# Performance work log

Measured on AMD Instinct MI355X. Metric: run time of the kernel, lower is better.

The kernel has to match this reference:

```python
import jax, jax.numpy as jnp
import numpy as np

TOP_K = 8
NUM_EXPERTS = 256
NUM_GROUPS = 8
TOPK_GROUP = 4
SCALE = 2.5
EPS = 1e-20


def setup_inputs() -> dict:
    key = jax.random.key(0)
    k1, k2, k3 = jax.random.split(key, 3)
    T, H = 8192, 7168
    hidden_states = jax.random.normal(k1, (T, H), dtype=jnp.float32)
    # scale ~ kaiming-ish so logits are O(1) and sigmoid is not saturated
    weight = jax.random.normal(k2, (NUM_EXPERTS, H), dtype=jnp.float32) * (H ** -0.5)
    e_score_correction_bias = jax.random.normal(k3, (NUM_EXPERTS,), dtype=jnp.float32) * 0.1
    return {"hidden_states": hidden_states, "weight": weight,
            "e_score_correction_bias": e_score_correction_bias}


def reference(hidden_states, weight, e_score_correction_bias):
    T = hidden_states.shape[0]
    epg = NUM_EXPERTS // NUM_GROUPS  # experts per group
    # gating logits: [T, E]
    logits = jnp.einsum('th,eh->te', hidden_states.astype(jnp.float32),
                        weight.astype(jnp.float32))
    scores = jax.nn.sigmoid(logits)
    scores_for_choice = scores + e_score_correction_bias[None, :]
    # group score = sum of top-2 corrected scores within each group: [T, G]
    grouped = scores_for_choice.reshape(T, NUM_GROUPS, epg)
    top2, _ = jax.lax.top_k(grouped, 2)
    group_scores = top2.sum(axis=-1)
    # select topk_group groups, build mask [T, G]
    _, group_idx = jax.lax.top_k(group_scores, TOPK_GROUP)
    group_mask = jnp.zeros((T, NUM_GROUPS), dtype=scores.dtype)
    group_mask = group_mask.at[jnp.arange(T)[:, None], group_idx].set(1.0)
    # expand to expert mask [T, E]
    score_mask = jnp.repeat(group_mask, epg, axis=1)
    tmp_scores = jnp.where(score_mask > 0, scores_for_choice, 0.0)
    # top_k experts among allowed groups
    _, topk_idx = jax.lax.top_k(tmp_scores, TOP_K)
    # gather UNcorrected scores as weights
    topk_weight = jnp.take_along_axis(scores, topk_idx, axis=1)
    topk_weight = topk_weight / (topk_weight.sum(axis=-1, keepdims=True) + EPS)
    topk_weight = topk_weight * SCALE
    return topk_idx, topk_weight
```

## Files before the change

### kernel.cpp

```cpp
#include <hip/hip_runtime.h>
#include <cmath>

typedef __attribute__((ext_vector_type(8))) _Float16 half8;
typedef __attribute__((ext_vector_type(8))) unsigned short ushort8;
typedef __attribute__((ext_vector_type(4))) float f32x4;

#define HH 7168
#define NE 256
#define NQ 224
#define NITER 112
#define TOPK 8
#define TOPKG 4
#define WSC 1024.f
#define INV_WS (1.f/1024.f)
#define C1 (1.f/2048.f)
#define C2 (1.f/4194304.f)

__device__ __forceinline__ void split2(float x, unsigned short& h, unsigned short& m){
  const _Float16 hh = (_Float16)x;
  const float r = x - (float)hh;
  const _Float16 mm = (_Float16)(r * 2048.f);
  h = __builtin_bit_cast(unsigned short, hh);
  m = __builtin_bit_cast(unsigned short, mm);
}

__global__ __launch_bounds__(256) void prep_w(const float* __restrict__ wgt,
                                              unsigned short* __restrict__ bh,
                                              unsigned short* __restrict__ bm){
  const int b = blockIdx.x;
  const int nt = b & 15, qb = (b >> 4) * 4;
  const int w = threadIdx.x >> 6, L = threadIdx.x & 63;
  const int q = qb + w;
  const int e = nt*16 + (L & 15);
  const int k0 = 32*q + 8*(L >> 4);
  const float4 a0 = *(const float4*)(wgt + (size_t)e*HH + k0);
  const float4 a1 = *(const float4*)(wgt + (size_t)e*HH + k0 + 4);
  const float v[8] = {a0.x,a0.y,a0.z,a0.w,a1.x,a1.y,a1.z,a1.w};
  ushort8 h8, m8;
#pragma unroll
  for(int j=0;j<8;j++){ unsigned short hh,mm; split2(v[j]*WSC, hh, mm); h8[j]=hh; m8[j]=mm; }
  const size_t base = ((size_t)(q*16+nt)*64 + L)*8;
  *(ushort8*)(bh+base) = h8;
  *(ushort8*)(bm+base) = m8;
}

#define ABYTE(buf,lvl,mt,q,row) ((((((buf)*2+(lvl))*2+(mt))*2+(q))*64+(row))*16)
#define BBYTE(buf,lvl,q,nt) ((((buf)*4+(lvl)*2+(q))*8+(nt))<<10)
__device__ __forceinline__ int swz(int bo){ return bo ^ (((bo >> 8) & 7) << 4); }

__device__ __forceinline__ void glds16(const void* g, void* l){
  __builtin_amdgcn_global_load_lds(
      (const __attribute__((address_space(1))) unsigned int*)g,
      (__attribute__((address_space(3))) unsigned int*)l, 16, 0, 0);
}

__global__ __launch_bounds__(512,4)
void gemm(const float* __restrict__ hs,
          const unsigned short* __restrict__ bhp,
          const unsigned short* __restrict__ bmp,
          float* __restrict__ lgout){
  __shared__ __align__(16) unsigned char blds[65536];
  __shared__ __align__(16) unsigned char alds[16384];

  const int tid = threadIdx.x, lane = tid & 63, w = tid >> 6;
  const int b = blockIdx.x;
  const int slice = (b >> 2) & 1;
  const int tg = (b >> 3)*4 + (b & 3);
  const int tb = tg*32, eb = slice*128;
  const int mtp = w >> 2, ntp = w & 3;

  f32x4 ksum[2], kcmp[2], c0[2], c1[2], c2[2];
#pragma unroll
  for(int c=0;c<2;c++){ ksum[c]=f32x4{0,0,0,0}; kcmp[c]=f32x4{0,0,0,0}; }

  const int tokS = (tid & 255) >> 3, kidx = tid & 7;
  const int mtS = tokS >> 4, m16S = tokS & 15;
  const int qS = kidx >> 2, kgS = kidx & 3;
  const int rowS = kgS*16 + m16S;
  const float* agp = hs + (size_t)(tb + tokS)*HH + kidx*8;

  auto stage = [&](int buf, const float4* g){
    unsigned short h[8], m[8];
    const float* gv = (const float*)g;
#pragma unroll
    for(int p=0;p<8;p++) split2(gv[p], h[p], m[p]);
    ushort8 h8, m8;
#pragma unroll
    for(int j=0;j<8;j++){ h8[j]=h[j]; m8[j]=m[j]; }
    *(ushort8*)&alds[swz(ABYTE(buf,0,mtS,qS,rowS))] = h8;
    *(ushort8*)&alds[swz(ABYTE(buf,1,mtS,qS,rowS))] = m8;
  };

  auto bstage = [&](int buf, int q32base){
#pragma unroll
    for(int j=0;j<4;j++){
      const int sid = w*4 + j;
      const int lvl = sid >> 4, q = (sid >> 3) & 1, nt = sid & 7;
      const int q32 = q32base + q;
      const unsigned short* src = (lvl ? bmp : bhp)
          + ((size_t)((q32*16 + slice*8 + nt)*64 + lane))*8;
      glds16(src, &blds[BBYTE(buf,lvl,q,nt)]);
    }
  };

  float4 ga[2];
  if(tid < 256){
    ga[0] = *(const float4*)(agp);
    ga[1] = *(const float4*)(agp + 4);
  }
  bstage(0, 0);
  if(tid < 256) stage(0, ga);
  __syncthreads();

  for(int i=0;i<NITER;i++){
    const int cur = i & 1, nb = cur ^ 1;
    const bool more = (i+1 < NITER);
    if(more){
      if(tid < 256){
        const float* ap = agp + (size_t)(i+1)*64;
        ga[0] = *(const float4*)(ap);
        ga[1] = *(const float4*)(ap + 4);
      }
      bstage(nb, 2*(i+1));
    }
    if((i & 1) == 0){
#pragma unroll
      for(int c=0;c<2;c++){ c0[c]=f32x4{0,0,0,0}; c1[c]=f32x4{0,0,0,0}; c2[c]=f32x4{0,0,0,0}; }
    }
#pragma unroll
    for(int s=0;s<2;s++){
      const half8 ah = *(const half8*)&alds[swz(ABYTE(cur,0,mtp,s,lane))];
      const half8 am = *(const half8*)&alds[swz(ABYTE(cur,1,mtp,s,lane))];
      half8 Bh[2], Bm[2];
#pragma unroll
      for(int ntl=0;ntl<2;ntl++){
        Bh[ntl] = *(const half8*)&blds[BBYTE(cur,0,s,ntp*2+ntl) + lane*16];
        Bm[ntl] = *(const half8*)&blds[BBYTE(cur,1,s,ntp*2+ntl) + lane*16];
      }
      __builtin_amdgcn_s_setprio(1);
#pragma unroll
      for(int ntl=0;ntl<2;ntl++){
        c0[ntl] = __builtin_amdgcn_mfma_f32_16x16x32_f16(ah, Bh[ntl], c0[ntl], 0,0,0);
        c1[ntl] = __builtin_amdgcn_mfma_f32_16x16x32_f16(ah, Bm[ntl], c1[ntl], 0,0,0);
        c1[ntl] = __builtin_amdgcn_mfma_f32_16x16x32_f16(am, Bh[ntl], c1[ntl], 0,0,0);
        c2[ntl] = __builtin_amdgcn_mfma_f32_16x16x32_f16(am, Bm[ntl], c2[ntl], 0,0,0);
      }
      __builtin_amdgcn_s_setprio(0);
    }
    if(more && tid < 256) stage(nb, ga);
    if(i & 1){
#pragma unroll
      for(int c=0;c<2;c++)
#pragma unroll
        for(int r=0;r<4;r++){
          const float v = c0[c][r] + c1[c][r]*C1 + c2[c][r]*C2;
          const float y = v - kcmp[c][r];
          const float t = ksum[c][r] + y;
          kcmp[c][r] = (t - ksum[c][r]) - y;
          ksum[c][r] = t;
        }
    }
    __syncthreads();
  }

#pragma unroll
  for(int ntl=0;ntl<2;ntl++)
#pragma unroll
    for(int r=0;r<4;r++){
      const int tok = mtp*16 + (lane>>4)*4 + r;
      const int e = (ntp*2+ntl)*16 + (lane&15);
      const float lg = (ksum[ntl][r] - kcmp[ntl][r]) * INV_WS;
      lgout[(size_t)(tb+tok)*NE + eb + e] = lg;
    }
}

__global__ __launch_bounds__(256)
void gate(const float* __restrict__ lg, const float* __restrict__ bias,
          float* __restrict__ out, int T){
  const int tid = threadIdx.x, lane = tid & 63, wv = tid >> 6;
  const int t = blockIdx.x*4 + wv;
  const float4 bias4 = *(const float4*)(bias + 4*lane);
  const int g = lane >> 3;
  const float NEG_INF = -__builtin_inff();

  const float4 l4 = *(const float4*)(lg + (size_t)t*NE + 4*lane);
  float4 r4;
  r4.x = 1.f/(1.f + expf(-l4.x));
  r4.y = 1.f/(1.f + expf(-l4.y));
  r4.z = 1.f/(1.f + expf(-l4.z));
  r4.w = 1.f/(1.f + expf(-l4.w));
  float4 s4;
  s4.x = r4.x + bias4.x; s4.y = r4.y + bias4.y;
  s4.z = r4.z + bias4.z; s4.w = r4.w + bias4.w;

  float m1 = s4.x, m2 = NEG_INF;
  if (s4.y > m1) { m2 = m1; m1 = s4.y; } else if (s4.y > m2) m2 = s4.y;
  if (s4.z > m1) { m2 = m1; m1 = s4.z; } else if (s4.z > m2) m2 = s4.z;
  if (s4.w > m1) { m2 = m1; m1 = s4.w; } else if (s4.w > m2) m2 = s4.w;
#pragma unroll
  for (int m = 1; m <= 4; m <<= 1) {
    const float o1 = __shfl_xor(m1, m);
    const float o2 = __shfl_xor(m2, m);
    const float nm1 = fmaxf(m1, o1);
    const float nm2 = fmaxf(fminf(m1, o1), fmaxf(m2, o2));
    m1 = nm1; m2 = nm2;
  }
  const float gs = m1 + m2;

  float gsv[8];
#pragma unroll
  for (int j = 0; j < 8; ++j) gsv[j] = __shfl(gs, j * 8);

  unsigned gm = 0;
#pragma unroll
  for (int r = 0; r < TOPKG; ++r) {
    float best = NEG_INF; int bj = 0;
#pragma unroll
    for (int j = 0; j < 8; ++j) {
      const bool avail = !((gm >> j) & 1u);
      if (avail && gsv[j] > best) { best = gsv[j]; bj = j; }
    }
    gm |= 1u << bj;
  }
  const bool allowed = (gm >> g) & 1u;

  float v0 = allowed ? s4.x : 0.f;
  float v1 = allowed ? s4.y : 0.f;
  float v2 = allowed ? s4.z : 0.f;
  float v3 = allowed ? s4.w : 0.f;

  float sumw = 0.f;
  int myidx = 0; float myraw = 0.f;
#pragma unroll
  for (int r = 0; r < TOPK; ++r) {
    float bv = v0; int bj = 0;
    if (v1 > bv) { bv = v1; bj = 1; }
    if (v2 > bv) { bv = v2; bj = 2; }
    if (v3 > bv) { bv = v3; bj = 3; }
    int bidx = 4 * lane + bj;
#pragma unroll
    for (int m = 1; m < 64; m <<= 1) {
      const float ov = __shfl_xor(bv, m);
      const int   oi = __shfl_xor(bidx, m);
      if (ov > bv || (ov == bv && oi < bidx)) { bv = ov; bidx = oi; }
    }
    const int oj = bidx & 3;
    const float cand = (oj == 0) ? r4.x
                     : (oj == 1) ? r4.y
                     : (oj == 2) ? r4.z
                     :             r4.w;
    const float raw = __shfl(cand, bidx >> 2);
    sumw += raw;
    if (lane == r) { myidx = bidx; myraw = raw; }
    if (lane == (bidx >> 2)) {
      if      (oj == 0) v0 = NEG_INF;
      else if (oj == 1) v1 = NEG_INF;
      else if (oj == 2) v2 = NEG_INF;
      else              v3 = NEG_INF;
    }
  }

  if (lane < TOPK) {
    out[(size_t)t * TOPK + lane] = (float)myidx;
    out[(size_t)T * TOPK + (size_t)t * TOPK + lane] = myraw / (sumw + 1e-20f) * 2.5f;
  }
}

extern "C" void kernel_launch(void* const* d_in, const int* in_sizes, int n_in,
                              void* d_out, int out_size, void* d_ws, size_t ws_size,
                              hipStream_t stream) {
  const float* hs   = (const float*)d_in[0];
  const float* wgt  = (const float*)d_in[1];
  const float* bias = (const float*)d_in[2];
  float* out = (float*)d_out;

  const int T = in_sizes[0] / HH;

  unsigned short* bh = (unsigned short*)d_ws;
  unsigned short* bm = bh + (size_t)NE*HH;
  float* lgbuf = (float*)(bm + (size_t)NE*HH);

  hipLaunchKernelGGL(prep_w, dim3(896), dim3(256), 0, stream, wgt, bh, bm);
  hipLaunchKernelGGL(gemm,   dim3(512), dim3(512), 0, stream, hs, bh, bm, lgbuf);
  hipLaunchKernelGGL(gate,   dim3(T/4), dim3(256), 0, stream, lgbuf, bias, out, T);
}
```

Baseline: 457.7 us.

## Double token tile per GEMM block to 64 with 2x2 MFMA tiles per wave

Each GEMM block now covers 64 tokens instead of 32. Each wave computes a 2x2 grid of 16x16 MFMA tiles, and all 512 threads participate in staging the A operand. This halves the number of blocks and the per-token traffic of the pre-split weight operand, raising arithmetic intensity per LDS/B load. The cost is more accumulator registers, a larger A LDS buffer, and fewer resident waves per CU (launch bounds lowered to 2), which reduces latency hiding.

```diff
diff --git a/kernel.cpp b/kernel.cpp
--- a/kernel.cpp
+++ b/kernel.cpp
@@ -44,8 +44,8 @@
   *(ushort8*)(bm+base) = m8;
 }
 
-#define ABYTE(buf,lvl,mt,q,row) ((((((buf)*2+(lvl))*2+(mt))*2+(q))*64+(row))*16)
-#define BBYTE(buf,lvl,q,nt) ((((buf)*4+(lvl)*2+(q))*8+(nt))<<10)
+#define AB(aw,lvl,mt,q,row) ((((((aw)*2+(lvl))*4+(mt))*2+(q))*64+(row))*16)
+#define BB(lvl,q,nt) ((((lvl)*2+(q))*8+(nt))<<10)
 __device__ __forceinline__ int swz(int bo){ return bo ^ (((bo >> 8) & 7) << 4); }
 
 __device__ __forceinline__ void glds16(const void* g, void* l){
@@ -54,124 +54,138 @@
       (__attribute__((address_space(3))) unsigned int*)l, 16, 0, 0);
 }
 
-__global__ __launch_bounds__(512,4)
+__global__ __launch_bounds__(512,2)
 void gemm(const float* __restrict__ hs,
           const unsigned short* __restrict__ bhp,
           const unsigned short* __restrict__ bmp,
           float* __restrict__ lgout){
   __shared__ __align__(16) unsigned char blds[65536];
-  __shared__ __align__(16) unsigned char alds[16384];
+  __shared__ __align__(16) unsigned char alds[32768];
 
   const int tid = threadIdx.x, lane = tid & 63, w = tid >> 6;
   const int b = blockIdx.x;
   const int slice = (b >> 2) & 1;
   const int tg = (b >> 3)*4 + (b & 3);
-  const int tb = tg*32, eb = slice*128;
+  const int tb = tg*64, eb = slice*128;
   const int mtp = w >> 2, ntp = w & 3;
 
-  f32x4 ksum[2], kcmp[2], c0[2], c1[2], c2[2];
-#pragma unroll
-  for(int c=0;c<2;c++){ ksum[c]=f32x4{0,0,0,0}; kcmp[c]=f32x4{0,0,0,0}; }
-
-  const int tokS = (tid & 255) >> 3, kidx = tid & 7;
+  f32x4 ksum[2][2], kcmp[2][2], c0[2][2], c1[2][2], c2[2][2];
+#pragma unroll
+  for(int a=0;a<2;a++)
+#pragma unroll
+    for(int c=0;c<2;c++){ ksum[a][c]=f32x4{0,0,0,0}; kcmp[a][c]=f32x4{0,0,0,0}; }
+
+  const int tokS = tid >> 3, kidx = tid & 7;
   const int mtS = tokS >> 4, m16S = tokS & 15;
   const int qS = kidx >> 2, kgS = kidx & 3;
   const int rowS = kgS*16 + m16S;
   const float* agp = hs + (size_t)(tb + tokS)*HH + kidx*8;
-
-  auto stage = [&](int buf, const float4* g){
+  float4 ga[2];
+
+  auto stage = [&](int aw){
     unsigned short h[8], m[8];
-    const float* gv = (const float*)g;
+    const float* gv = (const float*)ga;
 #pragma unroll
     for(int p=0;p<8;p++) split2(gv[p], h[p], m[p]);
     ushort8 h8, m8;
 #pragma unroll
     for(int j=0;j<8;j++){ h8[j]=h[j]; m8[j]=m[j]; }
-    *(ushort8*)&alds[swz(ABYTE(buf,0,mtS,qS,rowS))] = h8;
-    *(ushort8*)&alds[swz(ABYTE(buf,1,mtS,qS,rowS))] = m8;
+    *(ushort8*)&alds[swz(AB(aw,0,mtS,qS,rowS))] = h8;
+    *(ushort8*)&alds[swz(AB(aw,1,mtS,qS,rowS))] = m8;
   };
 
-  auto bstage = [&](int buf, int q32base){
+  auto bstage = [&](int bufoff, int inext){
 #pragma unroll
     for(int j=0;j<4;j++){
       const int sid = w*4 + j;
       const int lvl = sid >> 4, q = (sid >> 3) & 1, nt = sid & 7;
-      const int q32 = q32base + q;
+      const int q32 = 2*inext + q;
       const unsigned short* src = (lvl ? bmp : bhp)
           + ((size_t)((q32*16 + slice*8 + nt)*64 + lane))*8;
-      glds16(src, &blds[BBYTE(buf,lvl,q,nt)]);
+      glds16(src, &blds[bufoff + BB(lvl,q,nt)]);
     }
   };
 
-  float4 ga[2];
-  if(tid < 256){
-    ga[0] = *(const float4*)(agp);
-    ga[1] = *(const float4*)(agp + 4);
-  }
+  auto compute = [&](int aw, int s, int bbuf){
+    half8 ah[2], am[2];
+#pragma unroll
+    for(int mtl=0;mtl<2;mtl++){
+      const int mt = mtp*2 + mtl;
+      ah[mtl] = *(const half8*)&alds[swz(AB(aw,0,mt,s,lane))];
+      am[mtl] = *(const half8*)&alds[swz(AB(aw,1,mt,s,lane))];
+    }
+    half8 Bh[2], Bm[2];
+#pragma unroll
+    for(int ntl=0;ntl<2;ntl++){
+      Bh[ntl] = *(const half8*)&blds[bbuf + BB(0,s,ntp*2+ntl) + lane*16];
+      Bm[ntl] = *(const half8*)&blds[bbuf + BB(1,s,ntp*2+ntl) + lane*16];
+    }
+    __builtin_amdgcn_s_setprio(1);
+#pragma unroll
+    for(int mtl=0;mtl<2;mtl++)
+#pragma unroll
+      for(int ntl=0;ntl<2;ntl++){
+        c0[mtl][ntl] = __builtin_amdgcn_mfma_f32_16x16x32_f16(ah[mtl], Bh[ntl], c0[mtl][ntl], 0,0,0);
+        c1[mtl][ntl] = __builtin_amdgcn_mfma_f32_16x16x32_f16(ah[mtl], Bm[ntl], c1[mtl][ntl], 0,0,0);
+        c1[mtl][ntl] = __builtin_amdgcn_mfma_f32_16x16x32_f16(am[mtl], Bh[ntl], c1[mtl][ntl], 0,0,0);
+        c2[mtl][ntl] = __builtin_amdgcn_mfma_f32_16x16x32_f16(am[mtl], Bm[ntl], c2[mtl][ntl], 0,0,0);
+      }
+    __builtin_amdgcn_s_setprio(0);
+  };
+
+  ga[0] = *(const float4*)agp;
+  ga[1] = *(const float4*)(agp + 4);
   bstage(0, 0);
-  if(tid < 256) stage(0, ga);
+  stage(0);
   __syncthreads();
 
+#pragma unroll 1
   for(int i=0;i<NITER;i++){
     const int cur = i & 1, nb = cur ^ 1;
     const bool more = (i+1 < NITER);
     if(more){
-      if(tid < 256){
-        const float* ap = agp + (size_t)(i+1)*64;
-        ga[0] = *(const float4*)(ap);
-        ga[1] = *(const float4*)(ap + 4);
+      const float* ap = agp + (size_t)(i+1)*64;
+      ga[0] = *(const float4*)ap;
+      ga[1] = *(const float4*)(ap + 4);
+      bstage(nb*32768, i+1);
+    }
+    if((i & 1) == 0){
+#pragma unroll
+      for(int a=0;a<2;a++)
+#pragma unroll
+        for(int c=0;c<2;c++){ c0[a][c]=f32x4{0,0,0,0}; c1[a][c]=f32x4{0,0,0,0}; c2[a][c]=f32x4{0,0,0,0}; }
+    }
+    compute(cur, 0, cur*32768);
+    compute(cur, 1, cur*32768);
+    if(more) stage(nb);
+    if(i & 1){
+#pragma unroll
+      for(int a=0;a<2;a++)
+#pragma unroll
+        for(int c=0;c<2;c++)
+#pragma unroll
+          for(int r=0;r<4;r++){
+            const float v = c0[a][c][r] + c1[a][c][r]*C1 + c2[a][c][r]*C2;
+            const float y = v - kcmp[a][c][r];
+            const float t = ksum[a][c][r] + y;
+            kcmp[a][c][r] = (t - ksum[a][c][r]) - y;
+            ksum[a][c][r] = t;
+          }
+    }
+    __syncthreads();
+  }
+
+#pragma unroll
+  for(int mtl=0;mtl<2;mtl++)
+#pragma unroll
+    for(int ntl=0;ntl<2;ntl++)
+#pragma unroll
+      for(int r=0;r<4;r++){
+        const int tok = (mtp*2+mtl)*16 + (lane>>4)*4 + r;
+        const int e = (ntp*2+ntl)*16 + (lane&15);
+        const float lg = (ksum[mtl][ntl][r] - kcmp[mtl][ntl][r]) * INV_WS;
+        lgout[(size_t)(tb+tok)*NE + eb + e] = lg;
       }
-      bstage(nb, 2*(i+1));
-    }
-    if((i & 1) == 0){
-#pragma unroll
-      for(int c=0;c<2;c++){ c0[c]=f32x4{0,0,0,0}; c1[c]=f32x4{0,0,0,0}; c2[c]=f32x4{0,0,0,0}; }
-    }
-#pragma unroll
-    for(int s=0;s<2;s++){
-      const half8 ah = *(const half8*)&alds[swz(ABYTE(cur,0,mtp,s,lane))];
-      const half8 am = *(const half8*)&alds[swz(ABYTE(cur,1,mtp,s,lane))];
-      half8 Bh[2], Bm[2];
-#pragma unroll
-      for(int ntl=0;ntl<2;ntl++){
-        Bh[ntl] = *(const half8*)&blds[BBYTE(cur,0,s,ntp*2+ntl) + lane*16];
-        Bm[ntl] = *(const half8*)&blds[BBYTE(cur,1,s,ntp*2+ntl) + lane*16];
-      }
-      __builtin_amdgcn_s_setprio(1);
-#pragma unroll
-      for(int ntl=0;ntl<2;ntl++){
-        c0[ntl] = __builtin_amdgcn_mfma_f32_16x16x32_f16(ah, Bh[ntl], c0[ntl], 0,0,0);
-        c1[ntl] = __builtin_amdgcn_mfma_f32_16x16x32_f16(ah, Bm[ntl], c1[ntl], 0,0,0);
-        c1[ntl] = __builtin_amdgcn_mfma_f32_16x16x32_f16(am, Bh[ntl], c1[ntl], 0,0,0);
-        c2[ntl] = __builtin_amdgcn_mfma_f32_16x16x32_f16(am, Bm[ntl], c2[ntl], 0,0,0);
-      }
-      __builtin_amdgcn_s_setprio(0);
-    }
-    if(more && tid < 256) stage(nb, ga);
-    if(i & 1){
-#pragma unroll
-      for(int c=0;c<2;c++)
-#pragma unroll
-        for(int r=0;r<4;r++){
-          const float v = c0[c][r] + c1[c][r]*C1 + c2[c][r]*C2;
-          const float y = v - kcmp[c][r];
-          const float t = ksum[c][r] + y;
-          kcmp[c][r] = (t - ksum[c][r]) - y;
-          ksum[c][r] = t;
-        }
-    }
-    __syncthreads();
-  }
-
-#pragma unroll
-  for(int ntl=0;ntl<2;ntl++)
-#pragma unroll
-    for(int r=0;r<4;r++){
-      const int tok = mtp*16 + (lane>>4)*4 + r;
-      const int e = (ntp*2+ntl)*16 + (lane&15);
-      const float lg = (ksum[ntl][r] - kcmp[ntl][r]) * INV_WS;
-      lgout[(size_t)(tb+tok)*NE + eb + e] = lg;
-    }
 }
 
 __global__ __launch_bounds__(256)
@@ -281,6 +295,6 @@
   float* lgbuf = (float*)(bm + (size_t)NE*HH);
 
   hipLaunchKernelGGL(prep_w, dim3(896), dim3(256), 0, stream, wgt, bh, bm);
-  hipLaunchKernelGGL(gemm,   dim3(512), dim3(512), 0, stream, hs, bh, bm, lgbuf);
+  hipLaunchKernelGGL(gemm,   dim3(256), dim3(512), 0, stream, hs, bh, bm, lgbuf);
   hipLaunchKernelGGL(gate,   dim3(T/4), dim3(256), 0, stream, lgbuf, bias, out, T);
 }
```

Result: slower. 497.3 us (+8.7%).
